# Performance work log

Measured on AMD Instinct MI355X. Metric: run time of the kernel, lower is better.

Reference implementation:

```python
import jax, jax.numpy as jnp
import numpy as np

D_MODEL = 1024
N_HEADS = 16
HEAD_DIM = D_MODEL // N_HEADS  # 64; note: scores use full d_model dots but sqrt(head_dim) scale
WINDOW = 256
B, S = 4, 4096


def _window_starts(seq_len, ws):
    # replicate the torch loop: half-stride overlapping windows
    stride = ws // 2
    starts = []
    for i in range(0, seq_len, stride):
        end = min(i + ws, seq_len)
        start = max(0, end - ws)
        starts.append(start)
        if end == seq_len:
            break
    return np.asarray(starts, dtype=np.int32)


def setup_inputs() -> dict:
    key = jax.random.key(0)
    ks = jax.random.split(key, 9)
    sc = 0.02
    x = jax.random.normal(ks[0], (B, S, D_MODEL), dtype=jnp.float32)
    Wq = jax.random.normal(ks[1], (D_MODEL, D_MODEL), dtype=jnp.float32) * sc
    bq = jnp.zeros((D_MODEL,), jnp.float32)
    Wk = jax.random.normal(ks[2], (D_MODEL, D_MODEL), dtype=jnp.float32) * sc
    bk = jnp.zeros((D_MODEL,), jnp.float32)
    Wv = jax.random.normal(ks[3], (D_MODEL, D_MODEL), dtype=jnp.float32) * sc
    bv = jnp.zeros((D_MODEL,), jnp.float32)
    Wo = jax.random.normal(ks[4], (D_MODEL, D_MODEL), dtype=jnp.float32) * sc
    bo = jnp.zeros((D_MODEL,), jnp.float32)
    return {"x": x, "Wq": Wq, "bq": bq, "Wk": Wk, "bk": bk,
            "Wv": Wv, "bv": bv, "Wo": Wo, "bo": bo}


def reference(x, Wq, bq, Wk, bk, Wv, bv, Wo, bo):
    Bsz, seq, dm = x.shape
    q = x @ Wq + bq  # [B,S,D] (heads are re-flattened in the windowed path anyway)
    k = x @ Wk + bk
    v = x @ Wv + bv

    starts = _window_starts(seq, WINDOW)            # [W]
    idx = starts[:, None] + np.arange(WINDOW)[None]  # [W, ws] static indices
    idx_j = jnp.asarray(idx)

    qw = q[:, idx_j, :]  # [B, W, ws, D]
    kw = k[:, idx_j, :]
    vw = v[:, idx_j, :]

    scale = 1.0 / np.sqrt(HEAD_DIM).astype(np.float32)
    scores = jnp.einsum('bwid,bwjd->bwij', qw, kw) * scale  # full-d_model dots
    attn = jax.nn.softmax(scores, axis=-1)
    ow = jnp.einsum('bwij,bwjd->bwid', attn, vw)  # [B, W, ws, D]

    flat_idx = idx_j.reshape(-1)  # [W*ws]
    out = jnp.zeros_like(q).at[:, flat_idx, :].add(ow.reshape(Bsz, -1, dm))
    counts = jnp.zeros((seq,), jnp.float32).at[flat_idx].add(1.0)
    out = out / counts[None, :, None]  # overlap-add average

    return out @ Wo + bo
```

## Files before the change

### kernel.cpp

```cpp
#include <hip/hip_runtime.h>
#include <hip/hip_bf16.h>

typedef unsigned short u16;
typedef short bf16x8 __attribute__((ext_vector_type(8)));
typedef float f32x4 __attribute__((ext_vector_type(4)));

#define DM     1024
#define SEQ    4096
#define NBATCH 4
#define NWIN   31
#define NTOK   16384

__device__ __forceinline__ u16 f2b(float f) {
  union { float f; unsigned u; } x; x.f = f;
  unsigned r = (x.u + 0x7fffu + ((x.u >> 16) & 1u)) >> 16;
  return (u16)r;
}
__device__ __forceinline__ float b2f(u16 v) {
  union { unsigned u; float f; } x; x.u = ((unsigned)v) << 16; return x.f;
}
__device__ __forceinline__ void gload_lds16(const u16* g, u16* l) {
  __builtin_amdgcn_global_load_lds(
      (const __attribute__((address_space(1))) void*)g,
      (__attribute__((address_space(3))) void*)l, 16, 0, 0);
}

__global__ __launch_bounds__(256) void k_convert(const float* __restrict__ in,
                                                 u16* __restrict__ out, int n4) {
  int i = blockIdx.x * 256 + threadIdx.x;
  if (i >= n4) return;
  float4 v = ((const float4*)in)[i];
  ushort4 o; o.x = f2b(v.x); o.y = f2b(v.y); o.z = f2b(v.z); o.w = f2b(v.w);
  ((ushort4*)out)[i] = o;
}

__global__ __launch_bounds__(256) void k_transpose4(const float* __restrict__ W0,
                                                    const float* __restrict__ W1,
                                                    const float* __restrict__ W2,
                                                    const float* __restrict__ W3,
                                                    u16* __restrict__ Wt) {
  __shared__ float tile[32][33];
  int z = blockIdx.z;
  const float* W = (z == 0) ? W0 : (z == 1) ? W1 : (z == 2) ? W2 : W3;
  u16* dst = Wt + (size_t)z * DM * DM;
  int n0 = blockIdx.x * 32, k0 = blockIdx.y * 32;
  int tx = threadIdx.x, ty = threadIdx.y;
  #pragma unroll
  for (int i = ty; i < 32; i += 8) tile[i][tx] = W[(size_t)(k0 + i) * DM + n0 + tx];
  __syncthreads();
  #pragma unroll
  for (int i = ty; i < 32; i += 8) dst[(size_t)(n0 + i) * DM + k0 + tx] = f2b(tile[tx][i]);
}

__global__ __launch_bounds__(256) void k_catbias(const float* __restrict__ bq,
                                                 const float* __restrict__ bk,
                                                 const float* __restrict__ bv,
                                                 float* __restrict__ o) {
  int i = blockIdx.x * 256 + threadIdx.x;
  if (i >= 3 * DM) return;
  float v = (i < DM) ? bq[i] : (i < 2 * DM) ? bk[i - DM] : bv[i - 2 * DM];
  o[i] = v;
}

__global__ __launch_bounds__(512, 2) void k_gemm(const u16* __restrict__ A, const u16* __restrict__ Bt,
                                                 const float* __restrict__ bias,
                                                 float* __restrict__ Cf,
                                                 u16* __restrict__ Cb, int ldc,
                                                 u16* __restrict__ Ct, int csplit,
                                                 int M, int N, int K) {
  __shared__ u16 As[32768];
  __shared__ u16 Bs[32768];
  const int tid = threadIdx.x;
  const int wv = tid >> 6, lane = tid & 63;
  const int quad = lane >> 4, l16 = lane & 15;
  const int lr8 = lane >> 3;
  const int lc8 = (((lane & 7) ^ (lr8 & 7)) * 8);
  const int k7 = l16 & 7;

  const int nwg = gridDim.x * gridDim.y;
  const int orig = blockIdx.y * gridDim.x + blockIdx.x;
  const int swz = (orig & 7) * (nwg >> 3) + (orig >> 3);
  const int m0 = (swz / gridDim.x) * 256;
  const int n0 = (swz % gridDim.x) * 256;
  const int wm = wv >> 2, wn = wv & 3;
  const int bcol = (wn & 1) * 64;

  f32x4 acc[8][4];
  #pragma unroll
  for (int a = 0; a < 8; ++a)
    #pragma unroll
    for (int b = 0; b < 4; ++b) acc[a][b] = (f32x4){0.f, 0.f, 0.f, 0.f};

  const int nkt = K >> 6;
  const int send = nkt << 2;

#define STG(s_) do {                                                          \
    int s__ = (s_);                                                           \
    if (s__ < send) {                                                         \
      int ts__ = s__ >> 2, kd__ = s__ & 3;                                    \
      int cb__ = (ts__ & 1) << 14;                                            \
      int kk__ = ts__ << 6;                                                   \
      int e__ = wv * 2;                                                       \
      int row__ = e__ * 8 + lr8;                                              \
      if (kd__ == 0 || kd__ == 3) {                                           \
        int h__ = (kd__ == 3);                                                \
        gload_lds16(A + (size_t)(m0 + h__ * 128 + row__) * K + kk__ + lc8,    \
                    As + cb__ + h__ * 8192 + e__ * 512);                      \
        gload_lds16(A + (size_t)(m0 + h__ * 128 + row__ + 8) * K + kk__ + lc8,\
                    As + cb__ + h__ * 8192 + e__ * 512 + 512);                \
      } else {                                                                \
        int h__ = (kd__ == 2);                                                \
        gload_lds16(Bt + (size_t)(n0 + h__ * 128 + row__) * K + kk__ + lc8,   \
                    Bs + cb__ + h__ * 8192 + e__ * 512);                      \
        gload_lds16(Bt + (size_t)(n0 + h__ * 128 + row__ + 8) * K + kk__ + lc8,\
                    Bs + cb__ + h__ * 8192 + e__ * 512 + 512);                \
      }                                                                       \
    }                                                                         \
  } while (0)

#define RD_A(dst, mh) do {                                                    \
    _Pragma("unroll") for (int tt = 0; tt < 4; ++tt)                          \
    _Pragma("unroll") for (int s2 = 0; s2 < 2; ++s2)                          \
      dst[tt * 2 + s2] = *(const bf16x8*)&Aw[((mh) * 64 + tt * 16 + l16) * 64 \
                                             + (((s2 * 4 + quad) ^ k7) * 8)]; \
  } while (0)
#define RD_B(dst, nh) do {                                                    \
    _Pragma("unroll") for (int u = 0; u < 2; ++u)                             \
    _Pragma("unroll") for (int s2 = 0; s2 < 2; ++s2)                          \
      dst[u * 2 + s2] = *(const bf16x8*)&Bw[(bcol + (nh) * 32 + u * 16 + l16) * 64 \
                                            + (((s2 * 4 + quad) ^ k7) * 8)];  \
  } while (0)
#define MFQ(aarr, barr, mh, nh) do {                                          \
    __builtin_amdgcn_s_setprio(1);                                            \
    _Pragma("unroll") for (int s2 = 0; s2 < 2; ++s2)                          \
    _Pragma("unroll") for (int tt = 0; tt < 4; ++tt)                          \
    _Pragma("unroll") for (int u = 0; u < 2; ++u)                             \
      acc[(mh) * 4 + tt][(nh) * 2 + u] = __builtin_amdgcn_mfma_f32_16x16x32_bf16( \
          aarr[tt * 2 + s2], barr[u * 2 + s2], acc[(mh) * 4 + tt][(nh) * 2 + u], 0, 0, 0); \
    __builtin_amdgcn_s_setprio(0);                                            \
  } while (0)

  #pragma unroll
  for (int s = 0; s < 8; ++s) STG(s);
  asm volatile("s_waitcnt vmcnt(8)");
  __builtin_amdgcn_s_barrier();

  for (int t = 0; t < nkt; ++t) {
    const u16* Aw = As + ((t & 1) << 14) + wm * 8192;
    const u16* Bw = Bs + ((t & 1) << 14) + (wn >> 1) * 8192;
    bf16x8 a0[8], a1[8], b0[4], b1[4];

    RD_A(a0, 0); RD_B(b0, 0);
    __builtin_amdgcn_s_barrier();
    asm volatile("s_waitcnt lgkmcnt(0)");
    MFQ(a0, b0, 0, 0);
    __builtin_amdgcn_s_barrier();
    RD_A(a1, 1);
    __builtin_amdgcn_s_barrier();
    asm volatile("s_waitcnt lgkmcnt(0)");
    MFQ(a1, b0, 1, 0);
    __builtin_amdgcn_s_barrier();
    RD_B(b1, 1);
    STG(4 * (t + 2) + 0);
    STG(4 * (t + 2) + 3);
    __builtin_amdgcn_s_barrier();
    asm volatile("s_waitcnt lgkmcnt(0)");
    MFQ(a0, b1, 0, 1);
    __builtin_amdgcn_s_barrier();
    STG(4 * (t + 2) + 1);
    STG(4 * (t + 2) + 2);
    __builtin_amdgcn_s_barrier();
    MFQ(a1, b1, 1, 1);
    if (t < nkt - 2)       asm volatile("s_waitcnt vmcnt(8)");
    else if (t == nkt - 2) asm volatile("s_waitcnt vmcnt(0)");
    __builtin_amdgcn_s_barrier();
  }

#undef STG
#undef RD_A
#undef RD_B
#undef MFQ

  #pragma unroll
  for (int am = 0; am < 8; ++am) {
    #pragma unroll
    for (int an = 0; an < 4; ++an) {
      int row = m0 + wm * 128 + am * 16 + quad * 4;
      int col = n0 + wn * 64 + an * 16 + l16;
      float bv = bias[col];
      if (Cf) {
        #pragma unroll
        for (int r = 0; r < 4; ++r)
          Cf[(size_t)(row + r) * N + col] = acc[am][an][r] + bv;
      } else if (col < csplit) {
        #pragma unroll
        for (int r = 0; r < 4; ++r)
          Cb[(size_t)(row + r) * ldc + col] = f2b(acc[am][an][r] + bv);
      } else {
        ushort4 o;
        o.x = f2b(acc[am][an][0] + bv); o.y = f2b(acc[am][an][1] + bv);
        o.z = f2b(acc[am][an][2] + bv); o.w = f2b(acc[am][an][3] + bv);
        *(ushort4*)&Ct[(size_t)(col - csplit) * M + row] = o;
      }
    }
  }
}

#define LDQ  2048
__global__ __launch_bounds__(256, 2) void k_attn(const u16* __restrict__ QKb, const u16* __restrict__ Vt,
                                                 u16* __restrict__ oA, u16* __restrict__ oB) {
  __shared__ u16 stage[20480];
  __shared__ u16 Pbuf[64 * 256];
  __shared__ float red[2][4][64];
  u16* Qs = stage;
  u16* Ks = stage + 4096;
  u16* Vs = stage;

  const int tid = threadIdx.x;
  const int wv = tid >> 6, lane = tid & 63;
  const int quad = lane >> 4, l16 = lane & 15;
  const int l7 = lane & 7, lr8 = lane >> 3;
  const int kq = (l16 & 7) + (l16 >> 3);

  int id = blockIdx.x;
  int s_ = id >> 3;
  int qt = s_ & 3;
  int pair = (s_ >> 2) * 8 + (id & 7);
  if (pair >= NWIN * NBATCH) return;
  int b = pair / NWIN, w = pair - NWIN * b;

  const int s0 = w * 128;
  const size_t base2 = (size_t)b * SEQ * LDQ;
  const size_t base  = (size_t)b * SEQ * DM;
  const size_t btok  = (size_t)b * SEQ;
  const int qrow0 = s0 + qt * 64;

  f32x4 acc[4][4];
  #pragma unroll
  for (int mt = 0; mt < 4; ++mt)
    #pragma unroll
    for (int nt = 0; nt < 4; ++nt) acc[mt][nt] = (f32x4){0.f, 0.f, 0.f, 0.f};

  for (int kk = 0; kk < DM; kk += 64) {
    #pragma unroll
    for (int j = 0; j < 10; ++j) {
      int idx = wv * 10 + j;
      if (idx < 8) {
        int lc = (l7 ^ ((lr8 + idx) & 7)) * 8;
        gload_lds16(QKb + base2 + (size_t)(qrow0 + idx * 8 + lr8) * LDQ + kk + lc, Qs + idx * 512);
      } else {
        int f = idx - 8;
        int lc = (l7 ^ ((lr8 + f) & 7)) * 8;
        gload_lds16(QKb + DM + base2 + (size_t)(s0 + f * 8 + lr8) * LDQ + kk + lc, Ks + f * 512);
      }
    }
    __syncthreads();
    #pragma unroll
    for (int s2 = 0; s2 < 2; ++s2) {
      bf16x8 aq[4], bk[4];
      #pragma unroll
      for (int mt = 0; mt < 4; ++mt)
        aq[mt] = *(const bf16x8*)&Qs[(mt * 16 + l16) * 64 + (((s2 * 4 + quad) ^ ((kq + 2 * mt) & 7)) * 8)];
      #pragma unroll
      for (int nt = 0; nt < 4; ++nt)
        bk[nt] = *(const bf16x8*)&Ks[(wv * 64 + nt * 16 + l16) * 64 + (((s2 * 4 + quad) ^ ((kq + 2 * nt) & 7)) * 8)];
      #pragma unroll
      for (int mt = 0; mt < 4; ++mt)
        #pragma unroll
        for (int nt = 0; nt < 4; ++nt)
          acc[mt][nt] = __builtin_amdgcn_mfma_f32_16x16x32_bf16(aq[mt], bk[nt], acc[mt][nt], 0, 0, 0);
    }
    __syncthreads();
  }

  float mx[4][4], sm[4][4];
  #pragma unroll
  for (int mt = 0; mt < 4; ++mt)
    #pragma unroll
    for (int r = 0; r < 4; ++r) mx[mt][r] = -1e30f;
  #pragma unroll
  for (int mt = 0; mt < 4; ++mt)
    #pragma unroll
    for (int nt = 0; nt < 4; ++nt)
      #pragma unroll
      for (int r = 0; r < 4; ++r) {
        float v = acc[mt][nt][r] * 0.125f;
        acc[mt][nt][r] = v;
        mx[mt][r] = fmaxf(mx[mt][r], v);
      }
  #pragma unroll
  for (int mt = 0; mt < 4; ++mt)
    #pragma unroll
    for (int r = 0; r < 4; ++r)
      #pragma unroll
      for (int off = 8; off > 0; off >>= 1)
        mx[mt][r] = fmaxf(mx[mt][r], __shfl_xor(mx[mt][r], off, 64));
  if (l16 == 0) {
    #pragma unroll
    for (int mt = 0; mt < 4; ++mt)
      #pragma unroll
      for (int r = 0; r < 4; ++r)
        red[0][wv][mt * 16 + quad * 4 + r] = mx[mt][r];
  }
  __syncthreads();
  float gm[4][4];
  #pragma unroll
  for (int mt = 0; mt < 4; ++mt)
    #pragma unroll
    for (int r = 0; r < 4; ++r) {
      int q = mt * 16 + quad * 4 + r;
      gm[mt][r] = fmaxf(fmaxf(red[0][0][q], red[0][1][q]), fmaxf(red[0][2][q], red[0][3][q]));
      sm[mt][r] = 0.f;
    }
  #pragma unroll
  for (int mt = 0; mt < 4; ++mt)
    #pragma unroll
    for (int nt = 0; nt < 4; ++nt)
      #pragma unroll
      for (int r = 0; r < 4; ++r) {
        float e = __expf(acc[mt][nt][r] - gm[mt][r]);
        acc[mt][nt][r] = e;
        sm[mt][r] += e;
      }
  #pragma unroll
  for (int mt = 0; mt < 4; ++mt)
    #pragma unroll
    for (int r = 0; r < 4; ++r)
      #pragma unroll
      for (int off = 8; off > 0; off >>= 1)
        sm[mt][r] += __shfl_xor(sm[mt][r], off, 64);
  if (l16 == 0) {
    #pragma unroll
    for (int mt = 0; mt < 4; ++mt)
      #pragma unroll
      for (int r = 0; r < 4; ++r)
        red[1][wv][mt * 16 + quad * 4 + r] = sm[mt][r];
  }
  __syncthreads();
  #pragma unroll
  for (int mt = 0; mt < 4; ++mt)
    #pragma unroll
    for (int r = 0; r < 4; ++r) {
      int q = mt * 16 + quad * 4 + r;
      float inv = 1.f / (red[1][0][q] + red[1][1][q] + red[1][2][q] + red[1][3][q]);
      #pragma unroll
      for (int nt = 0; nt < 4; ++nt) {
        int ke = wv * 64 + nt * 16 + l16;
        int phys = (ke >> 3) ^ (q & 7);
        Pbuf[q * 256 + phys * 8 + (ke & 7)] = f2b(acc[mt][nt][r] * inv);
      }
    }
  __syncthreads();

  u16* op = ((w & 1) ? oB : oA) + base;
  for (int slab = 0; slab < 4; ++slab) {
    const int nb = slab * 256;
    f32x4 acc2[4][4];
    #pragma unroll
    for (int mt = 0; mt < 4; ++mt)
      #pragma unroll
      for (int u = 0; u < 4; ++u) acc2[mt][u] = (f32x4){0.f, 0.f, 0.f, 0.f};
    for (int sk = 0; sk < 4; ++sk) {
      const int tok0 = sk * 64;
      #pragma unroll
      for (int j = 0; j < 8; ++j) {
        int e = wv * 8 + j;
        int lc = (l7 ^ ((lr8 + e) & 7)) * 8;
        gload_lds16(Vt + (size_t)(nb + e * 8 + lr8) * NTOK + btok + s0 + tok0 + lc, Vs + e * 512);
      }
      __syncthreads();
      #pragma unroll
      for (int s2 = 0; s2 < 2; ++s2) {
        bf16x8 af[4];
        #pragma unroll
        for (int mt = 0; mt < 4; ++mt) {
          int cP = sk * 8 + s2 * 4 + quad;
          int phys = cP ^ (l16 & 7);
          af[mt] = *(const bf16x8*)&Pbuf[(mt * 16 + l16) * 256 + phys * 8];
        }
        #pragma unroll
        for (int u = 0; u < 4; ++u) {
          bf16x8 bb = *(const bf16x8*)&Vs[(wv * 64 + u * 16 + l16) * 64 +
                                          (((s2 * 4 + quad) ^ ((kq + 2 * u) & 7)) * 8)];
          #pragma unroll
          for (int mt = 0; mt < 4; ++mt)
            acc2[mt][u] = __builtin_amdgcn_mfma_f32_16x16x32_bf16(af[mt], bb, acc2[mt][u], 0, 0, 0);
        }
      }
      __syncthreads();
    }
    #pragma unroll
    for (int mt = 0; mt < 4; ++mt)
      #pragma unroll
      for (int u = 0; u < 4; ++u) {
        int row = qrow0 + mt * 16 + quad * 4;
        int col = nb + wv * 64 + u * 16 + l16;
        #pragma unroll
        for (int r = 0; r < 4; ++r)
          op[(size_t)(row + r) * DM + col] = f2b(acc2[mt][u][r]);
      }
  }
}

__global__ __launch_bounds__(256) void k_norm(const u16* __restrict__ oA, const u16* __restrict__ oB,
                                              u16* __restrict__ out, int n8) {
  int i = blockIdx.x * 256 + threadIdx.x;
  if (i >= n8) return;
  int s = (i >> 7) & (SEQ - 1);
  uint4 a = ((const uint4*)oA)[i];
  uint4 r = a;
  if (s >= 128 && s < 3968) {
    uint4 bq = ((const uint4*)oB)[i];
    const unsigned* ap = (const unsigned*)&a;
    const unsigned* bp = (const unsigned*)&bq;
    unsigned* rp = (unsigned*)&r;
    #pragma unroll
    for (int k = 0; k < 4; ++k) {
      float lo = 0.5f * (b2f((u16)(ap[k] & 0xffff)) + b2f((u16)(bp[k] & 0xffff)));
      float hi = 0.5f * (b2f((u16)(ap[k] >> 16))    + b2f((u16)(bp[k] >> 16)));
      rp[k] = (unsigned)f2b(lo) | ((unsigned)f2b(hi) << 16);
    }
  }
  ((uint4*)out)[i] = r;
}

extern "C" void kernel_launch(void* const* d_in, const int* in_sizes, int n_in,
                              void* d_out, int out_size, void* d_ws, size_t ws_size,
                              hipStream_t stream) {
  const float* x  = (const float*)d_in[0];
  const float* Wq = (const float*)d_in[1];
  const float* bq = (const float*)d_in[2];
  const float* Wk = (const float*)d_in[3];
  const float* bk = (const float*)d_in[4];
  const float* Wv = (const float*)d_in[5];
  const float* bv = (const float*)d_in[6];
  const float* Wo = (const float*)d_in[7];
  const float* bo = (const float*)d_in[8];
  float* out = (float*)d_out;

  char* ws = (char*)d_ws;
  const size_t MB = 1024 * 1024;
  u16*   xb   = (u16*)(ws);
  u16*   qkb  = (u16*)(ws + 32 * MB);
  u16*   vtb  = (u16*)(ws + 96 * MB);
  u16*   wqt  = (u16*)(ws + 128 * MB);
  float* bcat = (float*)(ws + 136 * MB);
  u16*   oA   = (u16*)(ws + 137 * MB);
  u16*   oB   = (u16*)(ws + 169 * MB);

  int n4tok = (int)((size_t)NTOK * DM / 4);
  k_convert<<<(n4tok + 255) / 256, 256, 0, stream>>>(x, xb, n4tok);
  k_transpose4<<<dim3(DM / 32, DM / 32, 4), dim3(32, 8), 0, stream>>>(Wq, Wk, Wv, Wo, wqt);
  k_catbias<<<12, 256, 0, stream>>>(bq, bk, bv, bcat);

  k_gemm<<<dim3(3 * DM / 256, NTOK / 256), 512, 0, stream>>>(
      xb, wqt, bcat, nullptr, qkb, 2048, vtb, 2048, NTOK, 3 * DM, DM);

  k_attn<<<512, 256, 0, stream>>>(qkb, vtb, oA, oB);

  int n8tok = (int)((size_t)NTOK * DM / 8);
  k_norm<<<(n8tok + 255) / 256, 256, 0, stream>>>(oA, oB, xb, n8tok);

  u16* wot = wqt + 3 * (size_t)DM * DM;
  k_gemm<<<dim3(DM / 256, NTOK / 256), 512, 0, stream>>>(
      xb, wot, bo, out, nullptr, DM, nullptr, DM, NTOK, DM, DM);
}
```

Before: 369.9 us.

## Fuse overlap-average into output projection GEMM and add MFMA priority hints

Removes the separate normalization kernel and folds the averaging of the two overlapping window outputs into the A-operand load of a new 128x128-tile output GEMM. The A tiles are loaded through registers, averaged, and written to swizzled LDS, while B is loaded directly to LDS. This drops one full write and read of the averaged activation buffer and one kernel launch. Separately, s_setprio is raised around the MFMA loops in the attention kernel. In exchange the GEMM reads both oA and oB for every tile and uses a smaller tile with no double buffering of the register-staged loads.

```diff
diff --git a/kernel.cpp b/kernel.cpp
--- a/kernel.cpp
+++ b/kernel.cpp
@@ -206,6 +206,100 @@
   }
 }
 
+__global__ __launch_bounds__(256, 4) void k_gemm_avg(const u16* __restrict__ oA,
+                                                     const u16* __restrict__ oB,
+                                                     const u16* __restrict__ Bt,
+                                                     const float* __restrict__ bias,
+                                                     float* __restrict__ Cf,
+                                                     int M, int N, int K) {
+  __shared__ u16 As[128 * 64];
+  __shared__ u16 Bs[128 * 64];
+  const int tid = threadIdx.x;
+  const int wv = tid >> 6, lane = tid & 63;
+  const int quad = lane >> 4, l16 = lane & 15;
+  const int lr8 = lane >> 3;
+  const int lc8 = (((lane & 7) ^ (lr8 & 7)) * 8);
+  const int m0 = blockIdx.y * 128, n0 = blockIdx.x * 128;
+  const int wm = (wv >> 1) * 64, wn = (wv & 1) * 64;
+  const int k7 = l16 & 7;
+  f32x4 acc[4][4];
+  #pragma unroll
+  for (int a = 0; a < 4; ++a)
+    #pragma unroll
+    for (int b = 0; b < 4; ++b) acc[a][b] = (f32x4){0.f, 0.f, 0.f, 0.f};
+
+  uint4 ra[4], rb[4];
+  int inter[4];
+
+#define LDA(kk_) do {                                                         \
+    _Pragma("unroll") for (int j = 0; j < 4; ++j) {                           \
+      int e = wv * 4 + j;                                                     \
+      int row = m0 + e * 8 + lr8;                                             \
+      int s = row & (SEQ - 1);                                                \
+      inter[j] = (s >= 128 && s < 3968);                                      \
+      size_t off = (size_t)row * K + (kk_) + lc8;                             \
+      ra[j] = *(const uint4*)&oA[off];                                        \
+      rb[j] = *(const uint4*)&oB[off];                                        \
+    }                                                                         \
+  } while (0)
+
+  LDA(0);
+  for (int kk = 0; kk < K; kk += 64) {
+    #pragma unroll
+    for (int j = 0; j < 4; ++j) {
+      int e = wv * 4 + j;
+      gload_lds16(Bt + (size_t)(n0 + e * 8 + lr8) * K + kk + lc8, Bs + e * 512);
+    }
+    #pragma unroll
+    for (int j = 0; j < 4; ++j) {
+      int e = wv * 4 + j;
+      uint4 a = ra[j], b = rb[j], o;
+      unsigned* ap = (unsigned*)&a;
+      unsigned* bp = (unsigned*)&b;
+      unsigned* op = (unsigned*)&o;
+      #pragma unroll
+      for (int w = 0; w < 4; ++w) {
+        float lo = 0.5f * (b2f((u16)(ap[w] & 0xffff)) + b2f((u16)(bp[w] & 0xffff)));
+        float hi = 0.5f * (b2f((u16)(ap[w] >> 16))    + b2f((u16)(bp[w] >> 16)));
+        op[w] = (unsigned)f2b(lo) | ((unsigned)f2b(hi) << 16);
+      }
+      if (!inter[j]) o = a;
+      *(uint4*)&As[e * 512 + lane * 8] = o;
+    }
+    if (kk + 64 < K) LDA(kk + 64);
+    __syncthreads();
+    #pragma unroll
+    for (int h = 0; h < 2; ++h) {
+      bf16x8 af[4], bfr[4];
+      #pragma unroll
+      for (int t = 0; t < 4; ++t)
+        af[t]  = *(const bf16x8*)&As[(wm + t * 16 + l16) * 64 + ((h * 4 + quad) ^ k7) * 8];
+      #pragma unroll
+      for (int t = 0; t < 4; ++t)
+        bfr[t] = *(const bf16x8*)&Bs[(wn + t * 16 + l16) * 64 + ((h * 4 + quad) ^ k7) * 8];
+      #pragma unroll
+      for (int mt = 0; mt < 4; ++mt)
+        #pragma unroll
+        for (int nt = 0; nt < 4; ++nt)
+          acc[mt][nt] = __builtin_amdgcn_mfma_f32_16x16x32_bf16(af[mt], bfr[nt], acc[mt][nt], 0, 0, 0);
+    }
+    __syncthreads();
+  }
+#undef LDA
+  #pragma unroll
+  for (int mt = 0; mt < 4; ++mt) {
+    #pragma unroll
+    for (int nt = 0; nt < 4; ++nt) {
+      int row = m0 + wm + mt * 16 + quad * 4;
+      int col = n0 + wn + nt * 16 + l16;
+      float bv = bias[col];
+      #pragma unroll
+      for (int r = 0; r < 4; ++r)
+        Cf[(size_t)(row + r) * N + col] = acc[mt][nt][r] + bv;
+    }
+  }
+}
+
 #define LDQ  2048
 __global__ __launch_bounds__(256, 2) void k_attn(const u16* __restrict__ QKb, const u16* __restrict__ Vt,
                                                  u16* __restrict__ oA, u16* __restrict__ oB) {
@@ -264,11 +358,13 @@
       #pragma unroll
       for (int nt = 0; nt < 4; ++nt)
         bk[nt] = *(const bf16x8*)&Ks[(wv * 64 + nt * 16 + l16) * 64 + (((s2 * 4 + quad) ^ ((kq + 2 * nt) & 7)) * 8)];
+      __builtin_amdgcn_s_setprio(1);
       #pragma unroll
       for (int mt = 0; mt < 4; ++mt)
         #pragma unroll
         for (int nt = 0; nt < 4; ++nt)
           acc[mt][nt] = __builtin_amdgcn_mfma_f32_16x16x32_bf16(aq[mt], bk[nt], acc[mt][nt], 0, 0, 0);
+      __builtin_amdgcn_s_setprio(0);
     }
     __syncthreads();
   }
@@ -382,9 +478,11 @@
         for (int u = 0; u < 4; ++u) {
           bf16x8 bb = *(const bf16x8*)&Vs[(wv * 64 + u * 16 + l16) * 64 +
                                           (((s2 * 4 + quad) ^ ((kq + 2 * u) & 7)) * 8)];
+          __builtin_amdgcn_s_setprio(1);
           #pragma unroll
           for (int mt = 0; mt < 4; ++mt)
             acc2[mt][u] = __builtin_amdgcn_mfma_f32_16x16x32_bf16(af[mt], bb, acc2[mt][u], 0, 0, 0);
+          __builtin_amdgcn_s_setprio(0);
         }
       }
       __syncthreads();
@@ -400,28 +498,6 @@
           op[(size_t)(row + r) * DM + col] = f2b(acc2[mt][u][r]);
       }
   }
-}
-
-__global__ __launch_bounds__(256) void k_norm(const u16* __restrict__ oA, const u16* __restrict__ oB,
-                                              u16* __restrict__ out, int n8) {
-  int i = blockIdx.x * 256 + threadIdx.x;
-  if (i >= n8) return;
-  int s = (i >> 7) & (SEQ - 1);
-  uint4 a = ((const uint4*)oA)[i];
-  uint4 r = a;
-  if (s >= 128 && s < 3968) {
-    uint4 bq = ((const uint4*)oB)[i];
-    const unsigned* ap = (const unsigned*)&a;
-    const unsigned* bp = (const unsigned*)&bq;
-    unsigned* rp = (unsigned*)&r;
-    #pragma unroll
-    for (int k = 0; k < 4; ++k) {
-      float lo = 0.5f * (b2f((u16)(ap[k] & 0xffff)) + b2f((u16)(bp[k] & 0xffff)));
-      float hi = 0.5f * (b2f((u16)(ap[k] >> 16))    + b2f((u16)(bp[k] >> 16)));
-      rp[k] = (unsigned)f2b(lo) | ((unsigned)f2b(hi) << 16);
-    }
-  }
-  ((uint4*)out)[i] = r;
 }
 
 extern "C" void kernel_launch(void* const* d_in, const int* in_sizes, int n_in,
@@ -458,10 +534,7 @@
 
   k_attn<<<512, 256, 0, stream>>>(qkb, vtb, oA, oB);
 
-  int n8tok = (int)((size_t)NTOK * DM / 8);
-  k_norm<<<(n8tok + 255) / 256, 256, 0, stream>>>(oA, oB, xb, n8tok);
-
   u16* wot = wqt + 3 * (size_t)DM * DM;
-  k_gemm<<<dim3(DM / 256, NTOK / 256), 512, 0, stream>>>(
-      xb, wot, bo, out, nullptr, DM, nullptr, DM, NTOK, DM, DM);
-}
+  k_gemm_avg<<<dim3(DM / 128, NTOK / 128), 256, 0, stream>>>(
+      oA, oB, wot, bo, out, NTOK, DM, DM);
+}
```

Result: slower. 605.4 us (+63.7%).
